# Optimization experiments

Hardware: AMD Instinct MI355X
Metric: run time of the kernel (lower is better)

## Reference

```python
import jax, jax.numpy as jnp
import numpy as np

N = 100000   # nodes
E = 1600000  # edges
F_IN, HID, OUT, K, L = 16, 128, 4, 3, 3


def setup_inputs() -> dict:
    key = jax.random.key(0)
    ks = jax.random.split(key, 16)
    x = jax.random.normal(ks[0], (N, F_IN), dtype=jnp.float32)
    edge_index = jax.random.randint(ks[1], (2, E), 0, N, dtype=jnp.int64)
    edge_attr = jax.random.uniform(ks[2], (E, 1), dtype=jnp.float32)
    s = 0.05
    # TAGConv l: K+1 stacked weight mats [K+1, in, out] + bias [out]
    W0 = jax.random.normal(ks[3], (K + 1, F_IN, HID), dtype=jnp.float32) * s
    b0 = jnp.zeros((HID,), dtype=jnp.float32)
    W1 = jax.random.normal(ks[4], (K + 1, HID, HID), dtype=jnp.float32) * s
    b1 = jnp.zeros((HID,), dtype=jnp.float32)
    W2 = jax.random.normal(ks[5], (K + 1, HID, HID), dtype=jnp.float32) * s
    b2 = jnp.zeros((HID,), dtype=jnp.float32)
    Wfc = jax.random.normal(ks[6], (HID, OUT), dtype=jnp.float32) * s
    bfc = jnp.zeros((OUT,), dtype=jnp.float32)
    return dict(x=x, edge_index=edge_index, edge_attr=edge_attr,
                W0=W0, b0=b0, W1=W1, b1=b1, W2=W2, b2=b2, Wfc=Wfc, bfc=bfc)


def _gcn_norm(row, col, edge_weight, num_nodes):
    # PyG gcn_norm with add_self_loops=False: deg over target (col)
    deg = jax.ops.segment_sum(edge_weight, col, num_segments=num_nodes)
    dis = jnp.where(deg > 0, 1.0 / jnp.sqrt(deg), 0.0)  # masked_fill inf -> 0
    return dis[row] * edge_weight * dis[col]  # [E]


def _tagconv(x, row, col, norm, W, b, num_nodes):
    # out = sum_k lin_k(A_norm^k x) + b
    out = x @ W[0]
    h = x
    for k in range(1, W.shape[0]):
        h = jax.ops.segment_sum(norm[:, None] * h[row], col, num_segments=num_nodes)
        out = out + h @ W[k]
    return out + b


def reference(x, edge_index, edge_attr, W0, b0, W1, b1, W2, b2, Wfc, bfc):
    row, col = edge_index[0], edge_index[1]
    ew = edge_attr.squeeze()
    norm = _gcn_norm(row, col, ew, N)
    h = x
    # layers 0..L-2: conv + (dropout p=0 identity) + relu
    for W, b in ((W0, b0), (W1, b1)):
        h = jax.nn.relu(_tagconv(h, row, col, norm, W, b, N))
    h = _tagconv(h, row, col, norm, W2, b2, N)
    return h @ Wfc + bfc
```

## Files before the change

### kernel.cpp

```cpp
#include <hip/hip_runtime.h>
#include <cstddef>
#include <cstdint>

#define NN 100000
#define NE 1600000

#define CB 1563
#define CBP 1568
#define EPB 4096
#define A1B 391

typedef unsigned short u16;
using short8 = __attribute__((ext_vector_type(8))) short;
using f32x4  = __attribute__((ext_vector_type(4))) float;

__device__ inline u16 f2bf(float f) {
    unsigned u = __float_as_uint(f);
    unsigned r = u + 0x7fffu + ((u >> 16) & 1u);
    return (u16)(r >> 16);
}
__device__ inline float bflo(unsigned u) { return __uint_as_float(u << 16); }
__device__ inline float bfhi(unsigned u) { return __uint_as_float(u & 0xffff0000u); }

__device__ inline float ew_of(unsigned p) { return __uint_as_float((p >> 17) << 16); }
__device__ inline int   src_of(unsigned p) { return (int)(p & 0x1FFFFu); }


__global__ __launch_bounds__(256) void hist_k(const int* __restrict__ col,
                                              unsigned* __restrict__ M) {
    __shared__ unsigned h[CBP];
    for (int i = threadIdx.x; i < CBP; i += 256) h[i] = 0;
    __syncthreads();
    int base = blockIdx.x * EPB;
    for (int i = threadIdx.x; i < EPB; i += 256) {
        int e = base + i;
        if (e < NE) atomicAdd(&h[col[e] >> 6], 1u);
    }
    __syncthreads();
    unsigned* mrow = M + (size_t)blockIdx.x * CBP;
    for (int i = threadIdx.x; i < CBP; i += 256) mrow[i] = h[i];
}

__global__ __launch_bounds__(256) void totals_k(const unsigned* __restrict__ M,
                                                unsigned* __restrict__ tot) {
    int b = blockIdx.x * 256 + threadIdx.x;
    if (b >= CBP) return;
    unsigned s = 0;
    for (int r = 0; r < A1B; ++r) s += M[(size_t)r * CBP + b];
    tot[b] = s;
}

__global__ __launch_bounds__(256) void scanb_k(const unsigned* __restrict__ tot,
                                               unsigned* __restrict__ cb) {
    __shared__ unsigned part[256];
    int t = threadIdx.x;
    unsigned loc[7];
    unsigned s = 0;
#pragma unroll
    for (int k = 0; k < 7; ++k) {
        int i = t * 7 + k;
        unsigned v = (i < CBP) ? tot[i] : 0;
        loc[k] = s; s += v;
    }
    part[t] = s;
    __syncthreads();
    for (int off = 1; off < 256; off <<= 1) {
        unsigned x = (t >= off) ? part[t - off] : 0;
        __syncthreads();
        part[t] += x;
        __syncthreads();
    }
    unsigned base = (t > 0) ? part[t - 1] : 0;
#pragma unroll
    for (int k = 0; k < 7; ++k) {
        int i = t * 7 + k;
        if (i <= CBP) cb[i] = base + loc[k];
    }
}

__global__ __launch_bounds__(256) void base_k(const unsigned* __restrict__ cb,
                                              unsigned* __restrict__ M) {
    int b = blockIdx.x * 256 + threadIdx.x;
    if (b >= CBP) return;
    unsigned run = cb[b];
    for (int r = 0; r < A1B; ++r) {
        unsigned v = M[(size_t)r * CBP + b];
        M[(size_t)r * CBP + b] = run;
        run += v;
    }
}

__global__ __launch_bounds__(256) void part_k(const int* __restrict__ row,
                                              const int* __restrict__ col,
                                              const float* __restrict__ ew,
                                              const unsigned* __restrict__ M,
                                              int2* __restrict__ Abuf) {
    __shared__ unsigned cur[CBP];
    const unsigned* mrow = M + (size_t)blockIdx.x * CBP;
    for (int i = threadIdx.x; i < CBP; i += 256) cur[i] = mrow[i];
    __syncthreads();
    int base = blockIdx.x * EPB;
    for (int i = threadIdx.x; i < EPB; i += 256) {
        int e = base + i;
        if (e < NE) {
            int c = col[e];
            unsigned pos = atomicAdd(&cur[c >> 6], 1u);
            Abuf[pos] = make_int2(row[e] | ((c & 63) << 17), __float_as_int(ew[e]));
        }
    }
}

__global__ __launch_bounds__(256) void build_k(const int2* __restrict__ Abuf,
                                               const unsigned* __restrict__ cb,
                                               int* __restrict__ rowptr,
                                               int2* __restrict__ epair,
                                               float* __restrict__ dis) {
    int b = blockIdx.x;
    int t = threadIdx.x;
    __shared__ int cnt[64];
    __shared__ int offs[64];
    __shared__ int ex[64];
    __shared__ float dsum[64];
    if (t < 64) { cnt[t] = 0; dsum[t] = 0.f; }
    __syncthreads();
    unsigned s = cb[b], e = cb[b + 1];
    int n = (int)(e - s);
    for (int i = t; i < n; i += 256) {
        int2 p = Abuf[s + i];
        int cl = (p.x >> 17) & 63;
        atomicAdd(&cnt[cl], 1);
        atomicAdd(&dsum[cl], __int_as_float(p.y));
    }
    __syncthreads();
    if (t < 64) offs[t] = cnt[t];
    __syncthreads();
    for (int off = 1; off < 64; off <<= 1) {
        int x = 0;
        if (t < 64 && t >= off) x = offs[t - off];
        __syncthreads();
        if (t < 64) offs[t] += x;
        __syncthreads();
    }
    if (t < 64) { ex[t] = offs[t] - cnt[t]; cnt[t] = 0; }
    __syncthreads();
    for (int i = t; i < n; i += 256) {
        int2 p = Abuf[s + i];
        int cl = (p.x >> 17) & 63;
        int r = atomicAdd(&cnt[cl], 1);
        epair[s + ex[cl] + r] = make_int2(p.x & 0x1FFFF, p.y);
    }
    if (t < 64) {
        int v = b * 64 + t;
        if (v < NN) {
            rowptr[v] = (int)s + ex[t];
            float d = dsum[t];
            dis[v] = (d > 0.f) ? (1.0f / sqrtf(d)) : 0.f;
        }
    }
    if (b == CB - 1 && t == 0) rowptr[NN] = NE;
}

__global__ void norm_k(const int* __restrict__ rowptr, const float* __restrict__ dis,
                       const int2* __restrict__ epair, unsigned* __restrict__ epc) {
    int v = blockIdx.x * 256 + threadIdx.x;
    if (v >= NN) return;
    float dv = dis[v];
    int s = rowptr[v], e = rowptr[v + 1];
    for (int i = s; i < e; ++i) {
        int2 p = epair[i];
        float w = dis[p.x] * __int_as_float(p.y) * dv;
        unsigned wb = (unsigned)f2bf(w) & 0x7FFFu;
        epc[i] = (wb << 17) | (unsigned)p.x;
    }
}

template <int K>
__global__ void wt_k(const float* __restrict__ W, u16* __restrict__ Wt) {
    int id = blockIdx.x * 256 + threadIdx.x;
    int j = id / K, k = id % K;
    Wt[(size_t)j * K + k] = f2bf(W[(size_t)k * 128 + j]);
}


__global__ void prop16_k(const float* __restrict__ hin, float* __restrict__ hout,
                         const int* __restrict__ rowptr, const unsigned* __restrict__ epc) {
    int t = blockIdx.x * 256 + threadIdx.x;
    int v = t >> 2, q = t & 3;
    if (v >= NN) return;
    int s = rowptr[v], e = rowptr[v + 1];
    const float* __restrict__ hq = hin + q * 4;
    float4 a0 = make_float4(0.f, 0.f, 0.f, 0.f);
    float4 a1 = make_float4(0.f, 0.f, 0.f, 0.f);
    int i = s;
    for (; i + 3 < e; i += 4) {
        unsigned p0 = epc[i], p1 = epc[i + 1], p2 = epc[i + 2], p3 = epc[i + 3];
        float4 h0 = *reinterpret_cast<const float4*>(hq + (size_t)src_of(p0) * 16);
        float4 h1 = *reinterpret_cast<const float4*>(hq + (size_t)src_of(p1) * 16);
        float4 h2 = *reinterpret_cast<const float4*>(hq + (size_t)src_of(p2) * 16);
        float4 h3 = *reinterpret_cast<const float4*>(hq + (size_t)src_of(p3) * 16);
        float w0 = ew_of(p0), w1 = ew_of(p1), w2 = ew_of(p2), w3 = ew_of(p3);
        a0.x += w0 * h0.x; a0.y += w0 * h0.y; a0.z += w0 * h0.z; a0.w += w0 * h0.w;
        a1.x += w1 * h1.x; a1.y += w1 * h1.y; a1.z += w1 * h1.z; a1.w += w1 * h1.w;
        a0.x += w2 * h2.x; a0.y += w2 * h2.y; a0.z += w2 * h2.z; a0.w += w2 * h2.w;
        a1.x += w3 * h3.x; a1.y += w3 * h3.y; a1.z += w3 * h3.z; a1.w += w3 * h3.w;
    }
    for (; i < e; ++i) {
        unsigned p = epc[i];
        float w = ew_of(p);
        float4 h = *reinterpret_cast<const float4*>(hq + (size_t)src_of(p) * 16);
        a0.x += w * h.x; a0.y += w * h.y; a0.z += w * h.z; a0.w += w * h.w;
    }
    float4 acc = make_float4(a0.x + a1.x, a0.y + a1.y, a0.z + a1.z, a0.w + a1.w);
    *reinterpret_cast<float4*>(hout + (size_t)v * 16 + q * 4) = acc;
}

__global__ void pack_k(const float* __restrict__ x, const float* __restrict__ p1,
                       const float* __restrict__ p2, const float* __restrict__ p3,
                       u16* __restrict__ Xcat) {
    int id = blockIdx.x * 256 + threadIdx.x;
    if (id >= NN * 4) return;
    int v = id >> 2, s = id & 3;
    const float* src = (s == 0 ? x : s == 1 ? p1 : s == 2 ? p2 : p3) + (size_t)v * 16;
    unsigned* dst = (unsigned*)(Xcat + (size_t)v * 64 + s * 16);
#pragma unroll
    for (int f = 0; f < 8; ++f) {
        dst[f] = (unsigned)f2bf(src[2 * f]) | ((unsigned)f2bf(src[2 * f + 1]) << 16);
    }
}

__global__ __launch_bounds__(256) void propbf_k(
    const u16* __restrict__ hin, u16* __restrict__ hout,
    const int* __restrict__ rowptr, const unsigned* __restrict__ epc) {
    int wid = (blockIdx.x * 256 + threadIdx.x) >> 6;
    int lane = threadIdx.x & 63;
    int g = lane >> 4;
    int l = lane & 15;
    int v = __builtin_amdgcn_readfirstlane(wid);
    int s = rowptr[v], e = rowptr[v + 1];
    const u16* __restrict__ hb = hin + l * 8;
    float a[8];
#pragma unroll
    for (int k = 0; k < 8; ++k) a[k] = 0.f;

    int i = s;
    for (; i + 7 < e; i += 8) {
        unsigned pa = epc[i + g];
        unsigned pb = epc[i + 4 + g];
        uint4 ha = *(const uint4*)(hb + (size_t)src_of(pa) * 512);
        uint4 hc = *(const uint4*)(hb + (size_t)src_of(pb) * 512);
        float wa = ew_of(pa), wb = ew_of(pb);
        a[0] += wa * bflo(ha.x); a[1] += wa * bfhi(ha.x);
        a[2] += wa * bflo(ha.y); a[3] += wa * bfhi(ha.y);
        a[4] += wa * bflo(ha.z); a[5] += wa * bfhi(ha.z);
        a[6] += wa * bflo(ha.w); a[7] += wa * bfhi(ha.w);
        a[0] += wb * bflo(hc.x); a[1] += wb * bfhi(hc.x);
        a[2] += wb * bflo(hc.y); a[3] += wb * bfhi(hc.y);
        a[4] += wb * bflo(hc.z); a[5] += wb * bfhi(hc.z);
        a[6] += wb * bflo(hc.w); a[7] += wb * bfhi(hc.w);
    }
    for (; i < e; i += 4) {
        int idx = i + g;
        unsigned p = (idx < e) ? epc[idx] : 0u;
        uint4 h = *(const uint4*)(hb + (size_t)src_of(p) * 512);
        float w = ew_of(p);
        a[0] += w * bflo(h.x); a[1] += w * bfhi(h.x);
        a[2] += w * bflo(h.y); a[3] += w * bfhi(h.y);
        a[4] += w * bflo(h.z); a[5] += w * bfhi(h.z);
        a[6] += w * bflo(h.w); a[7] += w * bfhi(h.w);
    }
#pragma unroll
    for (int k = 0; k < 8; ++k) {
        a[k] += __shfl_xor(a[k], 16);
        a[k] += __shfl_xor(a[k], 32);
    }
    if (g == 0) {
        uint4 o;
        o.x = (unsigned)f2bf(a[0]) | ((unsigned)f2bf(a[1]) << 16);
        o.y = (unsigned)f2bf(a[2]) | ((unsigned)f2bf(a[3]) << 16);
        o.z = (unsigned)f2bf(a[4]) | ((unsigned)f2bf(a[5]) << 16);
        o.w = (unsigned)f2bf(a[6]) | ((unsigned)f2bf(a[7]) << 16);
        *(uint4*)(hout + (size_t)v * 512 + l * 8) = o;
    }
}

template <int K, int RELU>
__global__ __launch_bounds__(512) void mgemm3_k(
    const u16* __restrict__ A, const u16* __restrict__ Bt,
    const float* __restrict__ bias, u16* __restrict__ outb) {
    const int NCH = K / 64;
    __shared__ u16 smB[2][64 * 128];
    int tid = threadIdx.x;
    int lane = tid & 63;
    int wv = tid >> 6;
    int r = lane & 15, h = lane >> 4;

    int v0 = blockIdx.x * 256 + wv * 32;
    bool active = v0 < NN;
    int arow0 = active ? v0 : 0;
    const u16* a0p = A + (size_t)(arow0 + r) * K + h * 8;
    const u16* a1p = a0p + (size_t)16 * K;

    float bj[8];
#pragma unroll
    for (int j = 0; j < 8; ++j) bj[j] = bias[j * 16 + r];

    int da = wv * 1024 + lane * 16;
    int db = da + 8192;
    int rowa = da >> 7, rowb = db >> 7;
    int sa = (da ^ ((rowa & 7) << 4)) & 127;
    int sb = (db ^ ((rowb & 7) << 4)) & 127;
    const char* gA = (const char*)Bt + (size_t)rowa * (2 * K) + sa;
    const char* gB = (const char*)Bt + (size_t)rowb * (2 * K) + sb;

    short8 ga = *(const short8*)(gA);
    short8 gb = *(const short8*)(gB);
    *(short8*)((char*)smB[0] + da) = ga;
    *(short8*)((char*)smB[0] + db) = gb;
    __syncthreads();

    f32x4 acc0[8], acc1[8];
#pragma unroll
    for (int j = 0; j < 8; ++j) {
        acc0[j] = {0.f, 0.f, 0.f, 0.f};
        acc1[j] = {0.f, 0.f, 0.f, 0.f};
    }

    int buf = 0;
    for (int c = 0; c < NCH; ++c) {
        if (c + 1 < NCH) {
            ga = *(const short8*)(gA + (c + 1) * 128);
            gb = *(const short8*)(gB + (c + 1) * 128);
        }
        const char* bbase = (const char*)smB[buf];
#pragma unroll
        for (int kk = 0; kk < 2; ++kk) {
            short8 a0 = *(const short8*)(a0p + c * 64 + kk * 32);
            short8 a1 = *(const short8*)(a1p + c * 64 + kk * 32);
#pragma unroll
            for (int j = 0; j < 8; ++j) {
                int bb = ((j * 16 + r) * 128 + kk * 64 + h * 16) ^ ((r & 7) << 4);
                short8 b = *(const short8*)(bbase + bb);
                acc0[j] = __builtin_amdgcn_mfma_f32_16x16x32_bf16(a0, b, acc0[j], 0, 0, 0);
                acc1[j] = __builtin_amdgcn_mfma_f32_16x16x32_bf16(a1, b, acc1[j], 0, 0, 0);
            }
        }
        if (c + 1 < NCH) {
            *(short8*)((char*)smB[buf ^ 1] + da) = ga;
            *(short8*)((char*)smB[buf ^ 1] + db) = gb;
        }
        __syncthreads();
        buf ^= 1;
    }

    if (active) {
#pragma unroll
        for (int i = 0; i < 4; ++i) {
            int row0 = v0 + h * 4 + i;
#pragma unroll
            for (int j = 0; j < 8; ++j) {
                float c0 = acc0[j][i] + bj[j];
                float c1 = acc1[j][i] + bj[j];
                if (RELU) { c0 = fmaxf(c0, 0.f); c1 = fmaxf(c1, 0.f); }
                outb[(size_t)row0 * 512 + j * 16 + r] = f2bf(c0);
                outb[(size_t)(row0 + 16) * 512 + j * 16 + r] = f2bf(c1);
            }
        }
    }
}

__global__ void fcb_k(const u16* __restrict__ H, const float* __restrict__ Wfc,
                      const float* __restrict__ bfc, float* __restrict__ out) {
    int t = blockIdx.x * 256 + threadIdx.x;
    int v = t >> 6, p = t & 63;
    unsigned u = *(const unsigned*)(H + (size_t)v * 512 + p * 2);
    float h0 = bflo(u), h1 = bfhi(u);
    float4 w0 = reinterpret_cast<const float4*>(Wfc)[2 * p];
    float4 w1 = reinterpret_cast<const float4*>(Wfc)[2 * p + 1];
    float s0 = h0 * w0.x + h1 * w1.x;
    float s1 = h0 * w0.y + h1 * w1.y;
    float s2 = h0 * w0.z + h1 * w1.z;
    float s3 = h0 * w0.w + h1 * w1.w;
#pragma unroll
    for (int off = 32; off; off >>= 1) {
        s0 += __shfl_xor(s0, off);
        s1 += __shfl_xor(s1, off);
        s2 += __shfl_xor(s2, off);
        s3 += __shfl_xor(s3, off);
    }
    if (p == 0) {
        float4 o = make_float4(s0 + bfc[0], s1 + bfc[1], s2 + bfc[2], s3 + bfc[3]);
        reinterpret_cast<float4*>(out)[v] = o;
    }
}


extern "C" void kernel_launch(void* const* d_in, const int* in_sizes, int n_in,
                              void* d_out, int out_size, void* d_ws, size_t ws_size,
                              hipStream_t stream) {
    const float* x    = (const float*)d_in[0];
    const int*   ei   = (const int*)d_in[1];
    const float* ea   = (const float*)d_in[2];
    const float* W0   = (const float*)d_in[3];
    const float* b0   = (const float*)d_in[4];
    const float* W1   = (const float*)d_in[5];
    const float* b1   = (const float*)d_in[6];
    const float* W2   = (const float*)d_in[7];
    const float* b2   = (const float*)d_in[8];
    const float* Wfc  = (const float*)d_in[9];
    const float* bfc  = (const float*)d_in[10];
    float* out = (float*)d_out;

    const int* row = ei;
    const int* col = ei + NE;

    char* w = (char*)d_ws;
    size_t off = 0;
    auto alloc = [&](size_t bytes) {
        size_t o = off;
        off += (bytes + 255) & ~(size_t)255;
        return (void*)(w + o);
    };
    int*      rowptr = (int*)     alloc((size_t)(NN + 1) * 4);
    float*    dis    = (float*)   alloc((size_t)NN * 4);
    unsigned* M      = (unsigned*)alloc((size_t)A1B * CBP * 4);
    unsigned* tot    = (unsigned*)alloc((size_t)CBP * 4);
    unsigned* cb     = (unsigned*)alloc((size_t)(CBP + 1) * 4);
    int2*     Abuf   = (int2*)    alloc((size_t)NE * 8);
    int2*     epair  = (int2*)    alloc((size_t)NE * 8);
    unsigned* epc    = (unsigned*)alloc((size_t)NE * 4);
    u16*      Wt0    = (u16*)     alloc((size_t)128 * 64 * 2);
    u16*      Wt1    = (u16*)     alloc((size_t)128 * 512 * 2);
    u16*      Wt2    = (u16*)     alloc((size_t)128 * 512 * 2);
    char*     ureg   = (char*)    alloc((size_t)NN * 128 * 4);
    float* P1   = (float*)(ureg);
    float* P2   = (float*)(ureg + (size_t)NN * 16 * 4);
    float* P3   = (float*)(ureg + (size_t)NN * 32 * 4);
    u16*   Xcat = (u16*)  (ureg + (size_t)NN * 48 * 4);
    u16*      Hcat   = (u16*)     alloc((size_t)NN * 512 * 2);
    (void)ws_size;

    const int nScanB = (NN + 255) / 256;
    const int nPropB = NN * 64 / 256;
    const int nTiles = (NN + 255) / 256;
    const int nBkt   = (CBP + 255) / 256;

    hist_k  <<<A1B,  256, 0, stream>>>(col, M);
    totals_k<<<nBkt, 256, 0, stream>>>(M, tot);
    scanb_k <<<1,    256, 0, stream>>>(tot, cb);
    base_k  <<<nBkt, 256, 0, stream>>>(cb, M);
    part_k  <<<A1B,  256, 0, stream>>>(row, col, ea, M, Abuf);
    build_k <<<CB,   256, 0, stream>>>(Abuf, cb, rowptr, epair, dis);
    norm_k  <<<nScanB, 256, 0, stream>>>(rowptr, dis, epair, epc);

    wt_k<64> <<<32,  256, 0, stream>>>(W0, Wt0);
    wt_k<512><<<256, 256, 0, stream>>>(W1, Wt1);
    wt_k<512><<<256, 256, 0, stream>>>(W2, Wt2);

    const int n16B = (NN * 4 + 255) / 256;
    prop16_k<<<n16B, 256, 0, stream>>>(x,  P1, rowptr, epc);
    prop16_k<<<n16B, 256, 0, stream>>>(P1, P2, rowptr, epc);
    prop16_k<<<n16B, 256, 0, stream>>>(P2, P3, rowptr, epc);
    pack_k<<<n16B, 256, 0, stream>>>(x, P1, P2, P3, Xcat);
    mgemm3_k<64, 1><<<nTiles, 512, 0, stream>>>(Xcat, Wt0, b0, Hcat);

    propbf_k<<<nPropB, 256, 0, stream>>>(Hcat,       Hcat + 128, rowptr, epc);
    propbf_k<<<nPropB, 256, 0, stream>>>(Hcat + 128, Hcat + 256, rowptr, epc);
    propbf_k<<<nPropB, 256, 0, stream>>>(Hcat + 256, Hcat + 384, rowptr, epc);
    mgemm3_k<512, 1><<<nTiles, 512, 0, stream>>>(Hcat, Wt1, b1, Hcat);

    propbf_k<<<nPropB, 256, 0, stream>>>(Hcat,       Hcat + 128, rowptr, epc);
    propbf_k<<<nPropB, 256, 0, stream>>>(Hcat + 128, Hcat + 256, rowptr, epc);
    propbf_k<<<nPropB, 256, 0, stream>>>(Hcat + 256, Hcat + 384, rowptr, epc);
    mgemm3_k<512, 0><<<nTiles, 512, 0, stream>>>(Hcat, Wt2, b2, Hcat);

    fcb_k<<<nPropB, 256, 0, stream>>>(Hcat, Wfc, bfc, out);
}
```

Measured before the change: 610.4 us.

## Propagate layer-0 features in bf16 in place and fuse final FC into GEMM epilogue

The first-layer propagation now runs in bf16 directly inside the concatenated Xcat buffer. It uses a wave-per-node gather over 8 edge groups, which removes the fp32 P1/P2/P3 buffers and the separate pack kernel. The last GEMM now applies the 128x4 fully connected layer in its epilogue, reducing across lanes with shuffles. This skips writing the final hidden state to memory, reading it back, and the separate fc kernel launch. The trade-off is extra bf16 rounding on the layer-0 propagated features and higher register pressure in the fused epilogue.

Measured after the change: 620.9 us. Within noise of the previous version (+1.7%).

```diff
diff --git a/kernel.cpp b/kernel.cpp
--- a/kernel.cpp
+++ b/kernel.cpp
@@ -182,49 +182,54 @@
 }
 
 
-__global__ void prop16_k(const float* __restrict__ hin, float* __restrict__ hout,
-                         const int* __restrict__ rowptr, const unsigned* __restrict__ epc) {
+__global__ void cvt16_k(const float* __restrict__ x, u16* __restrict__ Xcat) {
     int t = blockIdx.x * 256 + threadIdx.x;
-    int v = t >> 2, q = t & 3;
-    if (v >= NN) return;
+    if (t >= NN * 2) return;
+    int v = t >> 1, hf = t & 1;
+    const float* src = x + (size_t)v * 16 + hf * 8;
+    unsigned* dst = (unsigned*)(Xcat + (size_t)v * 64 + hf * 8);
+#pragma unroll
+    for (int f = 0; f < 4; ++f)
+        dst[f] = (unsigned)f2bf(src[2 * f]) | ((unsigned)f2bf(src[2 * f + 1]) << 16);
+}
+
+__global__ __launch_bounds__(256) void prop16b_k(
+    const u16* __restrict__ hin, u16* __restrict__ hout,
+    const int* __restrict__ rowptr, const unsigned* __restrict__ epc) {
+    int wid = (blockIdx.x * 256 + threadIdx.x) >> 6;
+    int lane = threadIdx.x & 63;
+    int g = lane >> 3;
+    int l = lane & 7;
+    int v = __builtin_amdgcn_readfirstlane(wid);
     int s = rowptr[v], e = rowptr[v + 1];
-    const float* __restrict__ hq = hin + q * 4;
-    float4 a0 = make_float4(0.f, 0.f, 0.f, 0.f);
-    float4 a1 = make_float4(0.f, 0.f, 0.f, 0.f);
+    const u16* __restrict__ hb = hin + l * 2;
+    float a0 = 0.f, a1 = 0.f, b0 = 0.f, b1 = 0.f;
     int i = s;
-    for (; i + 3 < e; i += 4) {
-        unsigned p0 = epc[i], p1 = epc[i + 1], p2 = epc[i + 2], p3 = epc[i + 3];
-        float4 h0 = *reinterpret_cast<const float4*>(hq + (size_t)src_of(p0) * 16);
-        float4 h1 = *reinterpret_cast<const float4*>(hq + (size_t)src_of(p1) * 16);
-        float4 h2 = *reinterpret_cast<const float4*>(hq + (size_t)src_of(p2) * 16);
-        float4 h3 = *reinterpret_cast<const float4*>(hq + (size_t)src_of(p3) * 16);
-        float w0 = ew_of(p0), w1 = ew_of(p1), w2 = ew_of(p2), w3 = ew_of(p3);
-        a0.x += w0 * h0.x; a0.y += w0 * h0.y; a0.z += w0 * h0.z; a0.w += w0 * h0.w;
-        a1.x += w1 * h1.x; a1.y += w1 * h1.y; a1.z += w1 * h1.z; a1.w += w1 * h1.w;
-        a0.x += w2 * h2.x; a0.y += w2 * h2.y; a0.z += w2 * h2.z; a0.w += w2 * h2.w;
-        a1.x += w3 * h3.x; a1.y += w3 * h3.y; a1.z += w3 * h3.z; a1.w += w3 * h3.w;
-    }
-    for (; i < e; ++i) {
-        unsigned p = epc[i];
+    for (; i + 15 < e; i += 16) {
+        unsigned pa = epc[i + g];
+        unsigned pb = epc[i + 8 + g];
+        unsigned ua = *(const unsigned*)(hb + (size_t)src_of(pa) * 64);
+        unsigned ub = *(const unsigned*)(hb + (size_t)src_of(pb) * 64);
+        float wa = ew_of(pa), wb = ew_of(pb);
+        a0 += wa * bflo(ua); a1 += wa * bfhi(ua);
+        b0 += wb * bflo(ub); b1 += wb * bfhi(ub);
+    }
+    for (; i < e; i += 8) {
+        int idx = i + g;
+        unsigned p = (idx < e) ? epc[idx] : 0u;
+        unsigned u = *(const unsigned*)(hb + (size_t)src_of(p) * 64);
         float w = ew_of(p);
-        float4 h = *reinterpret_cast<const float4*>(hq + (size_t)src_of(p) * 16);
-        a0.x += w * h.x; a0.y += w * h.y; a0.z += w * h.z; a0.w += w * h.w;
-    }
-    float4 acc = make_float4(a0.x + a1.x, a0.y + a1.y, a0.z + a1.z, a0.w + a1.w);
-    *reinterpret_cast<float4*>(hout + (size_t)v * 16 + q * 4) = acc;
-}
-
-__global__ void pack_k(const float* __restrict__ x, const float* __restrict__ p1,
-                       const float* __restrict__ p2, const float* __restrict__ p3,
-                       u16* __restrict__ Xcat) {
-    int id = blockIdx.x * 256 + threadIdx.x;
-    if (id >= NN * 4) return;
-    int v = id >> 2, s = id & 3;
-    const float* src = (s == 0 ? x : s == 1 ? p1 : s == 2 ? p2 : p3) + (size_t)v * 16;
-    unsigned* dst = (unsigned*)(Xcat + (size_t)v * 64 + s * 16);
-#pragma unroll
-    for (int f = 0; f < 8; ++f) {
-        dst[f] = (unsigned)f2bf(src[2 * f]) | ((unsigned)f2bf(src[2 * f + 1]) << 16);
+        a0 += w * bflo(u); a1 += w * bfhi(u);
+    }
+    a0 += b0; a1 += b1;
+#pragma unroll
+    for (int m = 8; m <= 32; m <<= 1) {
+        a0 += __shfl_xor(a0, m);
+        a1 += __shfl_xor(a1, m);
+    }
+    if (g == 0) {
+        *(unsigned*)(hout + (size_t)v * 64 + l * 2) =
+            (unsigned)f2bf(a0) | ((unsigned)f2bf(a1) << 16);
     }
 }
 
@@ -283,10 +288,12 @@
     }
 }
 
-template <int K, int RELU>
+template <int K, int RELU, int FC>
 __global__ __launch_bounds__(512) void mgemm3_k(
     const u16* __restrict__ A, const u16* __restrict__ Bt,
-    const float* __restrict__ bias, u16* __restrict__ outb) {
+    const float* __restrict__ bias, u16* __restrict__ outb,
+    const float* __restrict__ Wfc, const float* __restrict__ bfc,
+    float* __restrict__ outf) {
     const int NCH = K / 64;
     __shared__ u16 smB[2][64 * 128];
     int tid = threadIdx.x;
@@ -352,7 +359,9 @@
         buf ^= 1;
     }
 
-    if (active) {
+    if (!active) return;
+
+    if (!FC) {
 #pragma unroll
         for (int i = 0; i < 4; ++i) {
             int row0 = v0 + h * 4 + i;
@@ -365,31 +374,48 @@
                 outb[(size_t)(row0 + 16) * 512 + j * 16 + r] = f2bf(c1);
             }
         }
-    }
-}
-
-__global__ void fcb_k(const u16* __restrict__ H, const float* __restrict__ Wfc,
-                      const float* __restrict__ bfc, float* __restrict__ out) {
-    int t = blockIdx.x * 256 + threadIdx.x;
-    int v = t >> 6, p = t & 63;
-    unsigned u = *(const unsigned*)(H + (size_t)v * 512 + p * 2);
-    float h0 = bflo(u), h1 = bfhi(u);
-    float4 w0 = reinterpret_cast<const float4*>(Wfc)[2 * p];
-    float4 w1 = reinterpret_cast<const float4*>(Wfc)[2 * p + 1];
-    float s0 = h0 * w0.x + h1 * w1.x;
-    float s1 = h0 * w0.y + h1 * w1.y;
-    float s2 = h0 * w0.z + h1 * w1.z;
-    float s3 = h0 * w0.w + h1 * w1.w;
-#pragma unroll
-    for (int off = 32; off; off >>= 1) {
-        s0 += __shfl_xor(s0, off);
-        s1 += __shfl_xor(s1, off);
-        s2 += __shfl_xor(s2, off);
-        s3 += __shfl_xor(s3, off);
-    }
-    if (p == 0) {
-        float4 o = make_float4(s0 + bfc[0], s1 + bfc[1], s2 + bfc[2], s3 + bfc[3]);
-        reinterpret_cast<float4*>(out)[v] = o;
+    } else {
+        float4 wf[8];
+#pragma unroll
+        for (int j = 0; j < 8; ++j)
+            wf[j] = reinterpret_cast<const float4*>(Wfc)[j * 16 + r];
+        float p0[4][4], p1[4][4];
+#pragma unroll
+        for (int i = 0; i < 4; ++i)
+#pragma unroll
+            for (int o = 0; o < 4; ++o) { p0[i][o] = 0.f; p1[i][o] = 0.f; }
+#pragma unroll
+        for (int j = 0; j < 8; ++j) {
+#pragma unroll
+            for (int i = 0; i < 4; ++i) {
+                float c0 = acc0[j][i] + bj[j];
+                float c1 = acc1[j][i] + bj[j];
+                p0[i][0] += c0 * wf[j].x; p0[i][1] += c0 * wf[j].y;
+                p0[i][2] += c0 * wf[j].z; p0[i][3] += c0 * wf[j].w;
+                p1[i][0] += c1 * wf[j].x; p1[i][1] += c1 * wf[j].y;
+                p1[i][2] += c1 * wf[j].z; p1[i][3] += c1 * wf[j].w;
+            }
+        }
+#pragma unroll
+        for (int i = 0; i < 4; ++i)
+#pragma unroll
+            for (int o = 0; o < 4; ++o)
+#pragma unroll
+                for (int m = 1; m <= 8; m <<= 1) {
+                    p0[i][o] += __shfl_xor(p0[i][o], m);
+                    p1[i][o] += __shfl_xor(p1[i][o], m);
+                }
+        if (r == 0) {
+            float b0 = bfc[0], b1 = bfc[1], b2 = bfc[2], b3 = bfc[3];
+#pragma unroll
+            for (int i = 0; i < 4; ++i) {
+                int row0 = v0 + h * 4 + i;
+                reinterpret_cast<float4*>(outf)[row0] =
+                    make_float4(p0[i][0] + b0, p0[i][1] + b1, p0[i][2] + b2, p0[i][3] + b3);
+                reinterpret_cast<float4*>(outf)[row0 + 16] =
+                    make_float4(p1[i][0] + b0, p1[i][1] + b1, p1[i][2] + b2, p1[i][3] + b3);
+            }
+        }
     }
 }
 
@@ -431,11 +457,7 @@
     u16*      Wt0    = (u16*)     alloc((size_t)128 * 64 * 2);
     u16*      Wt1    = (u16*)     alloc((size_t)128 * 512 * 2);
     u16*      Wt2    = (u16*)     alloc((size_t)128 * 512 * 2);
-    char*     ureg   = (char*)    alloc((size_t)NN * 128 * 4);
-    float* P1   = (float*)(ureg);
-    float* P2   = (float*)(ureg + (size_t)NN * 16 * 4);
-    float* P3   = (float*)(ureg + (size_t)NN * 32 * 4);
-    u16*   Xcat = (u16*)  (ureg + (size_t)NN * 48 * 4);
+    u16*      Xcat   = (u16*)     alloc((size_t)NN * 64 * 2);
     u16*      Hcat   = (u16*)     alloc((size_t)NN * 512 * 2);
     (void)ws_size;
 
@@ -456,22 +478,22 @@
     wt_k<512><<<256, 256, 0, stream>>>(W1, Wt1);
     wt_k<512><<<256, 256, 0, stream>>>(W2, Wt2);
 
-    const int n16B = (NN * 4 + 255) / 256;
-    prop16_k<<<n16B, 256, 0, stream>>>(x,  P1, rowptr, epc);
-    prop16_k<<<n16B, 256, 0, stream>>>(P1, P2, rowptr, epc);
-    prop16_k<<<n16B, 256, 0, stream>>>(P2, P3, rowptr, epc);
-    pack_k<<<n16B, 256, 0, stream>>>(x, P1, P2, P3, Xcat);
-    mgemm3_k<64, 1><<<nTiles, 512, 0, stream>>>(Xcat, Wt0, b0, Hcat);
+    cvt16_k<<<(NN * 2 + 255) / 256, 256, 0, stream>>>(x, Xcat);
+    prop16b_k<<<nPropB, 256, 0, stream>>>(Xcat,      Xcat + 16, rowptr, epc);
+    prop16b_k<<<nPropB, 256, 0, stream>>>(Xcat + 16, Xcat + 32, rowptr, epc);
+    prop16b_k<<<nPropB, 256, 0, stream>>>(Xcat + 32, Xcat + 48, rowptr, epc);
+    mgemm3_k<64, 1, 0><<<nTiles, 512, 0, stream>>>(Xcat, Wt0, b0, Hcat,
+                                                   nullptr, nullptr, nullptr);
 
     propbf_k<<<nPropB, 256, 0, stream>>>(Hcat,       Hcat + 128, rowptr, epc);
     propbf_k<<<nPropB, 256, 0, stream>>>(Hcat + 128, Hcat + 256, rowptr, epc);
     propbf_k<<<nPropB, 256, 0, stream>>>(Hcat + 256, Hcat + 384, rowptr, epc);
-    mgemm3_k<512, 1><<<nTiles, 512, 0, stream>>>(Hcat, Wt1, b1, Hcat);
+    mgemm3_k<512, 1, 0><<<nTiles, 512, 0, stream>>>(Hcat, Wt1, b1, Hcat,
+                                                    nullptr, nullptr, nullptr);
 
     propbf_k<<<nPropB, 256, 0, stream>>>(Hcat,       Hcat + 128, rowptr, epc);
     propbf_k<<<nPropB, 256, 0, stream>>>(Hcat + 128, Hcat + 256, rowptr, epc);
     propbf_k<<<nPropB, 256, 0, stream>>>(Hcat + 256, Hcat + 384, rowptr, epc);
-    mgemm3_k<512, 0><<<nTiles, 512, 0, stream>>>(Hcat, Wt2, b2, Hcat);
-
-    fcb_k<<<nPropB, 256, 0, stream>>>(Hcat, Wfc, bfc, out);
-}
+    mgemm3_k<512, 0, 1><<<nTiles, 512, 0, stream>>>(Hcat, Wt2, b2, nullptr,
+                                                    Wfc, bfc, out);
+}
```
